# Kernel tuning notes

Measured on AMD Instinct MI355X. Metric: run time of the kernel, lower is better.

The kernel has to match this reference:

```python
import jax, jax.numpy as jnp
import numpy as np
from jax import lax


def setup_inputs() -> dict:
    key = jax.random.key(0)
    kx, kw = jax.random.split(key)
    x = jax.random.normal(kx, (32, 3, 8192), dtype=jnp.float32)
    weight = jax.random.normal(kw, (128, 3, 64), dtype=jnp.float32)
    return {"x": x, "weight": weight}


def reference(x, weight):
    # x: [B, C, L], weight: [O, C, K]
    K = weight.shape[2]
    # Cross-correlation (conv1d, no bias, valid padding): [B, O, L-K+1]
    conv_out = lax.conv_general_dilated(
        x, weight, window_strides=(1,), padding='VALID',
        dimension_numbers=('NCH', 'OIH', 'NCH'))
    # Half squared norm of each shapelet: [O]
    w_norm = jnp.sum(weight ** 2, axis=(1, 2)) / 2
    # Half squared norm of each length-K window, via cumulative sums
    # (avoids materializing the [B, C, W, K] unfold tensor)
    sq = jnp.sum(x ** 2, axis=1)               # [B, L]
    c = jnp.pad(jnp.cumsum(sq, axis=1), ((0, 0), (1, 0)))  # [B, L+1]
    win_norm = (c[:, K:] - c[:, :-K]) / 2      # [B, L-K+1]
    # features = conv_out - (||w||^2/2 + ||window||^2/2)
    features = conv_out - w_norm[None, :, None] - win_norm[:, None, :]
    # global max-pool over time, then *(-2) -> min squared distance
    return -2.0 * jnp.max(features, axis=-1)   # [B, O]
```

## Files before the change

### kernel.cpp

```cpp
#include <hip/hip_runtime.h>
#include <float.h>

#define BB 32
#define LL 8192
#define OO 128
#define KK 64
#define WW (LL - KK + 1)
#define NCH 4
#define GX 8

typedef __attribute__((ext_vector_type(8))) short short8;
typedef __attribute__((ext_vector_type(4))) float f32x4;

union AB { int4 i4; int i[4]; short8 v; };

static __device__ __forceinline__ unsigned int f2bf(float f) {
    unsigned int u = __builtin_bit_cast(unsigned int, f);
    return (u + 0x7FFFu + ((u >> 16) & 1u)) >> 16;
}

__global__ __launch_bounds__(256) void prep_kernel(const float* __restrict__ w,
                                                   unsigned short* __restrict__ wswz,
                                                   float* __restrict__ wn) {
    int g = blockIdx.x * 256 + threadIdx.x;
    if (g < 3072) {
        int ob = (g >= 1536) ? 1 : 0;
        int gg = g - ob * 1536;
        int ksqp = gg >> 6;
        int o2   = gg & 63;
        int ks = ksqp >> 2, qp = ksqp & 3;
        int c = ks >> 1, h = ks & 1;
        const float4* p = (const float4*)(w + (ob * 64 + o2) * 192 + c * 64 + h * 32 + qp * 8);
        float4 v0 = p[0], v1 = p[1];
        int4 pk;
        pk.x = (int)(f2bf(v0.x) | (f2bf(v0.y) << 16));
        pk.y = (int)(f2bf(v0.z) | (f2bf(v0.w) << 16));
        pk.z = (int)(f2bf(v1.x) | (f2bf(v1.y) << 16));
        pk.w = (int)(f2bf(v1.z) | (f2bf(v1.w) << 16));
        ((int4*)wswz)[g] = pk;
    }
    int oo = g - 3072;
    if (oo >= 0 && oo < OO) {
        const float* p = w + oo * 192;
        float s = 0.f;
        for (int i = 0; i < 192; ++i) { float v = p[i]; s = fmaf(v, v, s); }
        wn[oo] = 0.5f * s;
    }
}

static __device__ __forceinline__ void stage_chunk(const float* __restrict__ x, int b, int T0,
                                                   unsigned short* xl, float* sql, float* Pl,
                                                   int tid) {
    if (tid < 240) {
        int c = tid / 80, j4 = tid - c * 80;
        int l = T0 + j4 * 4;
        float4 v = make_float4(0.f, 0.f, 0.f, 0.f);
        if (l < LL) v = *(const float4*)(x + (b * 3 + c) * LL + l);
        uint2 pk;
        pk.x = f2bf(v.x) | (f2bf(v.y) << 16);
        pk.y = f2bf(v.z) | (f2bf(v.w) << 16);
        *(uint2*)(xl + c * 320 + j4 * 4) = pk;
    }
    {
        int l = T0 + tid;
        float s = 0.f;
        if (l < LL) {
            #pragma unroll
            for (int c = 0; c < 3; ++c) {
                float v = x[(b * 3 + c) * LL + l];
                s = fmaf(v, v, s);
            }
        }
        sql[tid] = s;
        float s8 = s + __shfl_xor(s, 1, 64);
        s8 += __shfl_xor(s8, 2, 64);
        s8 += __shfl_xor(s8, 4, 64);
        if ((tid & 7) == 0) Pl[tid >> 3] = s8;
    }
    if (tid < 64) {
        int j = 256 + tid, l = T0 + j;
        float s = 0.f;
        if (l < LL) {
            #pragma unroll
            for (int c = 0; c < 3; ++c) {
                float v = x[(b * 3 + c) * LL + l];
                s = fmaf(v, v, s);
            }
        }
        sql[j] = s;
        float s8 = s + __shfl_xor(s, 1, 64);
        s8 += __shfl_xor(s8, 2, 64);
        s8 += __shfl_xor(s8, 4, 64);
        if ((tid & 7) == 0) Pl[32 + (tid >> 3)] = s8;
    }
}

__global__ __launch_bounds__(256, 2) void shapeconv_main(const float* __restrict__ x,
                                                         const unsigned short* __restrict__ wswz,
                                                         const float* __restrict__ wn,
                                                         float* __restrict__ partial) {
    __shared__ __align__(16) unsigned short w_lds[64 * 192];
    __shared__ __align__(16) unsigned short x_lds[2][3 * 320];
    __shared__ __align__(16) float sq_lds[2][320];
    __shared__ float P_lds[2][40];
    __shared__ float win_lds[272];
    __shared__ float wn_lds[64];
    __shared__ float mred[64];

    const int tcx = blockIdx.x;
    const int ob = blockIdx.y;
    const int b  = blockIdx.z;
    const int tid = threadIdx.x;
    const int wv = tid >> 6;
    const int lane = tid & 63;
    const int wo = wv & 1, wt = wv >> 1;
    const int n  = lane & 15;
    const int qp = lane >> 4;
    const int Tb = tcx * (NCH * 256);

    {
        const char* src = (const char*)(wswz + ob * 1536 * 8) + tid * 16;
        #pragma unroll
        for (int i = 0; i < 6; ++i) {
            __builtin_amdgcn_global_load_lds(
                (const __attribute__((address_space(1))) unsigned int*)(src + i * 4096),
                (__attribute__((address_space(3))) unsigned int*)((char*)w_lds + wv * 1024 + i * 4096),
                16, 0, 0);
        }
    }
    if (tid < 64) wn_lds[tid] = wn[ob * 64 + tid];

    stage_chunk(x, b, Tb, x_lds[0], sq_lds[0], P_lds[0], tid);

    float m2[2][4];
    #pragma unroll
    for (int ot = 0; ot < 2; ++ot)
        #pragma unroll
        for (int rg = 0; rg < 4; ++rg) m2[ot][rg] = -FLT_MAX;

    for (int ci = 0; ci < NCH; ++ci) {
        const int bsel = ci & 1;
        const int T0 = Tb + ci * 256;
        __syncthreads();

        {
            int a = tid >> 3, bb2 = tid & 7;
            const float* sql = sq_lds[bsel];
            const float* Pl = P_lds[bsel];
            float s = 0.f;
            #pragma unroll
            for (int i = 1; i <= 7; ++i) s += Pl[a + i];
            #pragma unroll
            for (int k = 0; k < 8; ++k)
                s += (k >= bb2) ? sql[8 * a + k] : sql[8 * a + 64 + k];
            int pi = tid + (tid >> 4);
            win_lds[pi] = (T0 + tid < WW) ? 0.5f * s : 1e30f;
        }
        __syncthreads();

        f32x4 acc[2][8];
        {
            float wl[8];
            #pragma unroll
            for (int r = 0; r < 8; ++r) {
                int tl = 128 * wt + r + 8 * n;
                wl[r] = win_lds[tl + (tl >> 4)];
            }
            #pragma unroll
            for (int ot = 0; ot < 2; ++ot)
                #pragma unroll
                for (int rg = 0; rg < 4; ++rg) {
                    float nw = wn_lds[32 * wo + 16 * ot + 4 * qp + rg];
                    #pragma unroll
                    for (int r = 0; r < 8; ++r)
                        acc[ot][r][rg] = -nw - wl[r];
                }
        }

        if (ci + 1 < NCH)
            stage_chunk(x, b, T0 + 256, x_lds[1 - bsel], sq_lds[1 - bsel], P_lds[1 - bsel], tid);

        const char* xb = (const char*)x_lds[bsel];
        #pragma unroll
        for (int ks = 0; ks < 6; ++ks) {
            int c = ks >> 1, h = ks & 1;
            int e0b = c * 640 + 256 * wt + 64 * h + 16 * (n + qp);
            int4 Ea = *(const int4*)(xb + e0b);
            int4 Eb = *(const int4*)(xb + e0b + 16);
            int D[8] = {Ea.x, Ea.y, Ea.z, Ea.w, Eb.x, Eb.y, Eb.z, Eb.w};
            AB a0, a1;
            const int4* wq = (const int4*)w_lds + (ks * 4 + qp) * 64 + 32 * wo;
            a0.i4 = wq[n];
            a1.i4 = wq[16 + n];
            #pragma unroll
            for (int r = 0; r < 8; ++r) {
                AB bf;
                int s = r >> 1;
                if ((r & 1) == 0) {
                    bf.i[0] = D[s]; bf.i[1] = D[s + 1]; bf.i[2] = D[s + 2]; bf.i[3] = D[s + 3];
                } else {
                    #pragma unroll
                    for (int d = 0; d < 4; ++d)
                        bf.i[d] = (int)(((unsigned)D[s + d] >> 16) | ((unsigned)D[s + d + 1] << 16));
                }
                acc[0][r] = __builtin_amdgcn_mfma_f32_16x16x32_bf16(a0.v, bf.v, acc[0][r], 0, 0, 0);
                acc[1][r] = __builtin_amdgcn_mfma_f32_16x16x32_bf16(a1.v, bf.v, acc[1][r], 0, 0, 0);
            }
        }

        #pragma unroll
        for (int ot = 0; ot < 2; ++ot)
            #pragma unroll
            for (int rg = 0; rg < 4; ++rg) {
                float mm = m2[ot][rg];
                #pragma unroll
                for (int r = 0; r < 8; ++r) mm = fmaxf(mm, acc[ot][r][rg]);
                m2[ot][rg] = mm;
            }
    }

    #pragma unroll
    for (int s = 1; s <= 8; s <<= 1)
        #pragma unroll
        for (int ot = 0; ot < 2; ++ot)
            #pragma unroll
            for (int rg = 0; rg < 4; ++rg)
                m2[ot][rg] = fmaxf(m2[ot][rg], __shfl_xor(m2[ot][rg], s, 64));

    if (wt == 1 && n == 0) {
        #pragma unroll
        for (int ot = 0; ot < 2; ++ot)
            #pragma unroll
            for (int rg = 0; rg < 4; ++rg)
                mred[32 * wo + 16 * ot + 4 * qp + rg] = m2[ot][rg];
    }
    __syncthreads();
    if (wt == 0 && n == 0) {
        #pragma unroll
        for (int ot = 0; ot < 2; ++ot)
            #pragma unroll
            for (int rg = 0; rg < 4; ++rg) {
                int oi = 32 * wo + 16 * ot + 4 * qp + rg;
                float v = fmaxf(m2[ot][rg], mred[oi]);
                partial[((size_t)(b * GX + tcx) * 2 + ob) * 64 + oi] = v;
            }
    }
}

__global__ __launch_bounds__(256) void reduce_kernel(const float* __restrict__ partial,
                                                     float* __restrict__ out) {
    int idx = blockIdx.x * 256 + threadIdx.x;
    int b = idx >> 7, o = idx & 127;
    const float* pp = partial + ((size_t)b * GX * 2 + (o >> 6)) * 64 + (o & 63);
    float mx = -FLT_MAX;
    #pragma unroll
    for (int t = 0; t < GX; ++t) mx = fmaxf(mx, pp[(size_t)t * 128]);
    out[idx] = -2.f * mx;
}

extern "C" void kernel_launch(void* const* d_in, const int* in_sizes, int n_in,
                              void* d_out, int out_size, void* d_ws, size_t ws_size,
                              hipStream_t stream) {
    const float* x = (const float*)d_in[0];
    const float* w = (const float*)d_in[1];
    float* out = (float*)d_out;

    unsigned short* wswz = (unsigned short*)d_ws;
    float* wn = (float*)((char*)d_ws + 49152);
    float* partial = (float*)((char*)d_ws + 49664);

    prep_kernel<<<13, 256, 0, stream>>>(w, wswz, wn);
    dim3 grid(GX, 2, BB);
    shapeconv_main<<<grid, 256, 0, stream>>>(x, wswz, wn, partial);
    reduce_kernel<<<16, 256, 0, stream>>>(partial, out);
}
```

Before: 74.81 us.

## Fuse weight prep into main kernel, register-prefetch x, recompute window norms per lane

Drops the separate prep kernel: each block converts its weight half to bf16 and computes weight norms itself. Input chunks are loaded into registers early and written to LDS after the MFMA loop, which removes two barriers per chunk and the shared window-norm buffer. Window norms are now computed per lane with a sliding sum. The grid is reshaped to 11 column blocks of 3 chunks with 3 blocks per CU, and MFMA sections raise wave priority. The trade-off is redundant weight conversion in every block and more register pressure.

```diff
diff --git a/kernel.cpp b/kernel.cpp
--- a/kernel.cpp
+++ b/kernel.cpp
@@ -6,8 +6,8 @@
 #define OO 128
 #define KK 64
 #define WW (LL - KK + 1)
-#define NCH 4
-#define GX 8
+#define NCH 3
+#define GX 11
 
 typedef __attribute__((ext_vector_type(8))) short short8;
 typedef __attribute__((ext_vector_type(4))) float f32x4;
@@ -19,92 +19,51 @@
     return (u + 0x7FFFu + ((u >> 16) & 1u)) >> 16;
 }
 
-__global__ __launch_bounds__(256) void prep_kernel(const float* __restrict__ w,
-                                                   unsigned short* __restrict__ wswz,
-                                                   float* __restrict__ wn) {
-    int g = blockIdx.x * 256 + threadIdx.x;
-    if (g < 3072) {
-        int ob = (g >= 1536) ? 1 : 0;
-        int gg = g - ob * 1536;
-        int ksqp = gg >> 6;
-        int o2   = gg & 63;
-        int ks = ksqp >> 2, qp = ksqp & 3;
-        int c = ks >> 1, h = ks & 1;
-        const float4* p = (const float4*)(w + (ob * 64 + o2) * 192 + c * 64 + h * 32 + qp * 8);
-        float4 v0 = p[0], v1 = p[1];
-        int4 pk;
-        pk.x = (int)(f2bf(v0.x) | (f2bf(v0.y) << 16));
-        pk.y = (int)(f2bf(v0.z) | (f2bf(v0.w) << 16));
-        pk.z = (int)(f2bf(v1.x) | (f2bf(v1.y) << 16));
-        pk.w = (int)(f2bf(v1.z) | (f2bf(v1.w) << 16));
-        ((int4*)wswz)[g] = pk;
-    }
-    int oo = g - 3072;
-    if (oo >= 0 && oo < OO) {
-        const float* p = w + oo * 192;
-        float s = 0.f;
-        for (int i = 0; i < 192; ++i) { float v = p[i]; s = fmaf(v, v, s); }
-        wn[oo] = 0.5f * s;
-    }
-}
-
-static __device__ __forceinline__ void stage_chunk(const float* __restrict__ x, int b, int T0,
-                                                   unsigned short* xl, float* sql, float* Pl,
-                                                   int tid) {
-    if (tid < 240) {
-        int c = tid / 80, j4 = tid - c * 80;
-        int l = T0 + j4 * 4;
-        float4 v = make_float4(0.f, 0.f, 0.f, 0.f);
-        if (l < LL) v = *(const float4*)(x + (b * 3 + c) * LL + l);
+static __device__ __forceinline__ void stage_load(const float* __restrict__ x, int b, int T0,
+                                                  int tid, float4* v) {
+    v[0] = make_float4(0.f, 0.f, 0.f, 0.f);
+    v[1] = v[0];
+    v[2] = v[0];
+    if (tid < 80) {
+        int l = T0 + 4 * tid;
+        if (l < LL) {
+            const float* p = x + (size_t)b * 3 * LL + l;
+            v[0] = *(const float4*)(p);
+            v[1] = *(const float4*)(p + LL);
+            v[2] = *(const float4*)(p + 2 * LL);
+        }
+    }
+}
+
+static __device__ __forceinline__ void stage_store(int tid, const float4* v,
+                                                   unsigned short* xl, float* sql, float* Pl) {
+    if (tid >= 80) return;
+    #pragma unroll
+    for (int c = 0; c < 3; ++c) {
         uint2 pk;
-        pk.x = f2bf(v.x) | (f2bf(v.y) << 16);
-        pk.y = f2bf(v.z) | (f2bf(v.w) << 16);
-        *(uint2*)(xl + c * 320 + j4 * 4) = pk;
-    }
-    {
-        int l = T0 + tid;
-        float s = 0.f;
-        if (l < LL) {
-            #pragma unroll
-            for (int c = 0; c < 3; ++c) {
-                float v = x[(b * 3 + c) * LL + l];
-                s = fmaf(v, v, s);
-            }
-        }
-        sql[tid] = s;
-        float s8 = s + __shfl_xor(s, 1, 64);
-        s8 += __shfl_xor(s8, 2, 64);
-        s8 += __shfl_xor(s8, 4, 64);
-        if ((tid & 7) == 0) Pl[tid >> 3] = s8;
-    }
-    if (tid < 64) {
-        int j = 256 + tid, l = T0 + j;
-        float s = 0.f;
-        if (l < LL) {
-            #pragma unroll
-            for (int c = 0; c < 3; ++c) {
-                float v = x[(b * 3 + c) * LL + l];
-                s = fmaf(v, v, s);
-            }
-        }
-        sql[j] = s;
-        float s8 = s + __shfl_xor(s, 1, 64);
-        s8 += __shfl_xor(s8, 2, 64);
-        s8 += __shfl_xor(s8, 4, 64);
-        if ((tid & 7) == 0) Pl[32 + (tid >> 3)] = s8;
-    }
-}
-
-__global__ __launch_bounds__(256, 2) void shapeconv_main(const float* __restrict__ x,
-                                                         const unsigned short* __restrict__ wswz,
-                                                         const float* __restrict__ wn,
+        pk.x = f2bf(v[c].x) | (f2bf(v[c].y) << 16);
+        pk.y = f2bf(v[c].z) | (f2bf(v[c].w) << 16);
+        *(uint2*)(xl + c * 320 + tid * 4) = pk;
+    }
+    float4 sq4;
+    sq4.x = fmaf(v[2].x, v[2].x, fmaf(v[1].x, v[1].x, v[0].x * v[0].x));
+    sq4.y = fmaf(v[2].y, v[2].y, fmaf(v[1].y, v[1].y, v[0].y * v[0].y));
+    sq4.z = fmaf(v[2].z, v[2].z, fmaf(v[1].z, v[1].z, v[0].z * v[0].z));
+    sq4.w = fmaf(v[2].w, v[2].w, fmaf(v[1].w, v[1].w, v[0].w * v[0].w));
+    *(float4*)(sql + tid * 4) = sq4;
+    float s4 = (sq4.x + sq4.y) + (sq4.z + sq4.w);
+    float s8 = s4 + __shfl_xor(s4, 1, 64);
+    if ((tid & 1) == 0) Pl[tid >> 1] = s8;
+}
+
+__global__ __launch_bounds__(256, 3) void shapeconv_main(const float* __restrict__ x,
+                                                         const float* __restrict__ w,
                                                          float* __restrict__ partial) {
     __shared__ __align__(16) unsigned short w_lds[64 * 192];
     __shared__ __align__(16) unsigned short x_lds[2][3 * 320];
     __shared__ __align__(16) float sq_lds[2][320];
-    __shared__ float P_lds[2][40];
-    __shared__ float win_lds[272];
-    __shared__ float wn_lds[64];
+    __shared__ __align__(16) float P_lds[2][40];
+    __shared__ float wnp[4][64];
     __shared__ float mred[64];
 
     const int tcx = blockIdx.x;
@@ -118,19 +77,47 @@
     const int qp = lane >> 4;
     const int Tb = tcx * (NCH * 256);
 
+    float4 sv[3];
+    stage_load(x, b, Tb, tid, sv);
+
     {
-        const char* src = (const char*)(wswz + ob * 1536 * 8) + tid * 16;
+        const int o2 = tid & 63;
+        const int row = tid >> 6;
+        const float* wb = w + ((size_t)(ob * 64 + o2)) * 192;
+        float wsq = 0.f;
         #pragma unroll
         for (int i = 0; i < 6; ++i) {
-            __builtin_amdgcn_global_load_lds(
-                (const __attribute__((address_space(1))) unsigned int*)(src + i * 4096),
-                (__attribute__((address_space(3))) unsigned int*)((char*)w_lds + wv * 1024 + i * 4096),
-                16, 0, 0);
-        }
-    }
-    if (tid < 64) wn_lds[tid] = wn[ob * 64 + tid];
-
-    stage_chunk(x, b, Tb, x_lds[0], sq_lds[0], P_lds[0], tid);
+            int g = tid + 256 * i;
+            int ksqp = g >> 6;
+            int ks = ksqp >> 2, qq = ksqp & 3;
+            int c = ks >> 1, h = ks & 1;
+            const float4* p = (const float4*)(wb + c * 64 + h * 32 + qq * 8);
+            float4 v0 = p[0], v1 = p[1];
+            int4 pk;
+            pk.x = (int)(f2bf(v0.x) | (f2bf(v0.y) << 16));
+            pk.y = (int)(f2bf(v0.z) | (f2bf(v0.w) << 16));
+            pk.z = (int)(f2bf(v1.x) | (f2bf(v1.y) << 16));
+            pk.w = (int)(f2bf(v1.z) | (f2bf(v1.w) << 16));
+            ((int4*)w_lds)[g] = pk;
+            wsq = fmaf(v0.x, v0.x, wsq); wsq = fmaf(v0.y, v0.y, wsq);
+            wsq = fmaf(v0.z, v0.z, wsq); wsq = fmaf(v0.w, v0.w, wsq);
+            wsq = fmaf(v1.x, v1.x, wsq); wsq = fmaf(v1.y, v1.y, wsq);
+            wsq = fmaf(v1.z, v1.z, wsq); wsq = fmaf(v1.w, v1.w, wsq);
+        }
+        wnp[row][o2] = wsq;
+    }
+
+    stage_store(tid, sv, x_lds[0], sq_lds[0], P_lds[0]);
+    __syncthreads();
+
+    float nw[2][4];
+    #pragma unroll
+    for (int ot = 0; ot < 2; ++ot)
+        #pragma unroll
+        for (int rg = 0; rg < 4; ++rg) {
+            int o = 32 * wo + 16 * ot + 4 * qp + rg;
+            nw[ot][rg] = 0.5f * ((wnp[0][o] + wnp[1][o]) + (wnp[2][o] + wnp[3][o]));
+        }
 
     float m2[2][4];
     #pragma unroll
@@ -141,46 +128,35 @@
     for (int ci = 0; ci < NCH; ++ci) {
         const int bsel = ci & 1;
         const int T0 = Tb + ci * 256;
-        __syncthreads();
-
+        const bool more = (ci + 1 < NCH);
+        if (more) stage_load(x, b, T0 + 256, tid, sv);
+
+        float wl[8];
         {
-            int a = tid >> 3, bb2 = tid & 7;
-            const float* sql = sq_lds[bsel];
-            const float* Pl = P_lds[bsel];
-            float s = 0.f;
-            #pragma unroll
-            for (int i = 1; i <= 7; ++i) s += Pl[a + i];
-            #pragma unroll
-            for (int k = 0; k < 8; ++k)
-                s += (k >= bb2) ? sql[8 * a + k] : sql[8 * a + 64 + k];
-            int pi = tid + (tid >> 4);
-            win_lds[pi] = (T0 + tid < WW) ? 0.5f * s : 1e30f;
-        }
-        __syncthreads();
+            const float* sqp = sq_lds[bsel];
+            const float* Pl  = P_lds[bsel];
+            const int mi = 16 * wt + n;
+            float S = 0.f;
+            #pragma unroll
+            for (int i = 0; i < 8; ++i) S += Pl[mi + i];
+            #pragma unroll
+            for (int r = 0; r < 8; ++r) {
+                wl[r] = (T0 + 8 * mi + r < WW) ? 0.5f * S : 1e30f;
+                if (r < 7) S += sqp[8 * mi + 64 + r] - sqp[8 * mi + r];
+            }
+        }
 
         f32x4 acc[2][8];
-        {
-            float wl[8];
-            #pragma unroll
-            for (int r = 0; r < 8; ++r) {
-                int tl = 128 * wt + r + 8 * n;
-                wl[r] = win_lds[tl + (tl >> 4)];
-            }
-            #pragma unroll
-            for (int ot = 0; ot < 2; ++ot)
+        #pragma unroll
+        for (int ot = 0; ot < 2; ++ot)
+            #pragma unroll
+            for (int rg = 0; rg < 4; ++rg)
                 #pragma unroll
-                for (int rg = 0; rg < 4; ++rg) {
-                    float nw = wn_lds[32 * wo + 16 * ot + 4 * qp + rg];
-                    #pragma unroll
-                    for (int r = 0; r < 8; ++r)
-                        acc[ot][r][rg] = -nw - wl[r];
-                }
-        }
-
-        if (ci + 1 < NCH)
-            stage_chunk(x, b, T0 + 256, x_lds[1 - bsel], sq_lds[1 - bsel], P_lds[1 - bsel], tid);
+                for (int r = 0; r < 8; ++r)
+                    acc[ot][r][rg] = -nw[ot][rg] - wl[r];
 
         const char* xb = (const char*)x_lds[bsel];
+        __builtin_amdgcn_s_setprio(1);
         #pragma unroll
         for (int ks = 0; ks < 6; ++ks) {
             int c = ks >> 1, h = ks & 1;
@@ -207,6 +183,7 @@
                 acc[1][r] = __builtin_amdgcn_mfma_f32_16x16x32_bf16(a1.v, bf.v, acc[1][r], 0, 0, 0);
             }
         }
+        __builtin_amdgcn_s_setprio(0);
 
         #pragma unroll
         for (int ot = 0; ot < 2; ++ot)
@@ -217,6 +194,11 @@
                 for (int r = 0; r < 8; ++r) mm = fmaxf(mm, acc[ot][r][rg]);
                 m2[ot][rg] = mm;
             }
+
+        if (more) {
+            stage_store(tid, sv, x_lds[1 - bsel], sq_lds[1 - bsel], P_lds[1 - bsel]);
+            __syncthreads();
+        }
     }
 
     #pragma unroll
@@ -265,12 +247,9 @@
     const float* w = (const float*)d_in[1];
     float* out = (float*)d_out;
 
-    unsigned short* wswz = (unsigned short*)d_ws;
-    float* wn = (float*)((char*)d_ws + 49152);
-    float* partial = (float*)((char*)d_ws + 49664);
-
-    prep_kernel<<<13, 256, 0, stream>>>(w, wswz, wn);
+    float* partial = (float*)d_ws;
+
     dim3 grid(GX, 2, BB);
-    shapeconv_main<<<grid, 256, 0, stream>>>(x, wswz, wn, partial);
+    shapeconv_main<<<grid, 256, 0, stream>>>(x, w, partial);
     reduce_kernel<<<16, 256, 0, stream>>>(partial, out);
 }
```

After: 72.92 us. 2.5% less time.
